# Kernel tuning notes

Measured on AMD Instinct MI355X. Metric: run time of the kernel, lower is better.

Reference implementation:

```python
import jax, jax.numpy as jnp
import numpy as np

B, T, C = 4, 2048, 2048  # batch, n_target, n_context
KEY_SIZE = 1024
VALUE_SIZE = 1024
NUM_HEADS = 16
KEY_HIDDEN = 64
HEAD_SIZE = VALUE_SIZE // NUM_HEADS  # 64
NORMALISE = True


def setup_inputs() -> dict:
    key = jax.random.key(0)
    ks = jax.random.split(key, 7)
    s = 0.02
    return {
        "queries": jax.random.normal(ks[0], (B, T, KEY_SIZE), jnp.float32),
        "keys": jax.random.normal(ks[1], (B, C, KEY_SIZE), jnp.float32),
        "values": jax.random.normal(ks[2], (B, C, VALUE_SIZE), jnp.float32),
        "Wq": jax.random.normal(ks[3], (NUM_HEADS * KEY_HIDDEN, KEY_SIZE), jnp.float32) * s,
        "Wk": jax.random.normal(ks[4], (NUM_HEADS * KEY_HIDDEN, KEY_SIZE), jnp.float32) * s,
        "Wv": jax.random.normal(ks[5], (NUM_HEADS * HEAD_SIZE, VALUE_SIZE), jnp.float32) * s,
        "Wo": jax.random.normal(ks[6], (VALUE_SIZE, NUM_HEADS * HEAD_SIZE), jnp.float32) * s,
    }


def reference(queries, keys, values, Wq, Wk, Wv, Wo):
    # Linear projections (torch nn.Linear: x @ W.T), reshape to heads
    q = (queries @ Wq.T).reshape(B, T, NUM_HEADS, KEY_HIDDEN)   # [B,T,H,Dk]
    k = (keys @ Wk.T).reshape(B, C, NUM_HEADS, KEY_HIDDEN)      # [B,C,H,Dk]
    v = (values @ Wv.T).reshape(B, C, NUM_HEADS, HEAD_SIZE)     # [B,C,H,Dv]
    scale = np.sqrt(KEY_HIDDEN).astype(np.float32)
    # Scores [B,H,T,C]
    scores = jnp.einsum('bthd,bchd->bhtc', q, k) / scale
    if NORMALISE:
        attn = jax.nn.softmax(scores, axis=-1)
    else:
        attn = jax.nn.sigmoid(scores)
    out = jnp.einsum('bhtc,bchd->bthd', attn, v)                # [B,T,H,Dv]
    out = out.reshape(B, T, NUM_HEADS * HEAD_SIZE)
    return out @ Wo.T                                            # [B,T,VALUE_SIZE]
```

## Files before the change

kernel.cpp:

```cpp
#include <hip/hip_runtime.h>
#include <stdint.h>

#define BATCH 4
#define SEQ   2048
#define EMB   1024
#define NH    16
#define HD    64

typedef __attribute__((ext_vector_type(4))) float  floatx4;
typedef __attribute__((ext_vector_type(8))) short  shortx8;

__device__ __forceinline__ unsigned short f2bf(float f) {
  unsigned u = __builtin_bit_cast(unsigned, f);
  u += 0x7FFFu + ((u >> 16) & 1u);
  return (unsigned short)(u >> 16);
}

__device__ __forceinline__ unsigned pack2bf(float a, float b) {
  return (unsigned)f2bf(a) | ((unsigned)f2bf(b) << 16);
}

__device__ __forceinline__ unsigned packtrunc(float a, float b) {
#if __has_builtin(__builtin_amdgcn_perm)
  return __builtin_amdgcn_perm(__builtin_bit_cast(unsigned, b),
                               __builtin_bit_cast(unsigned, a), 0x07060302u);
#else
  return (__builtin_bit_cast(unsigned, a) >> 16) |
         (__builtin_bit_cast(unsigned, b) & 0xFFFF0000u);
#endif
}

__device__ __forceinline__ float fexp2(float x) {
#if __has_builtin(__builtin_amdgcn_exp2f)
  return __builtin_amdgcn_exp2f(x);
#else
  return exp2f(x);
#endif
}

__device__ __forceinline__ void gl_lds16(const void* g, void* l) {
  __builtin_amdgcn_global_load_lds((const __attribute__((address_space(1))) void*)g,
                                   (__attribute__((address_space(3))) void*)l,
                                   16, 0, 0);
}

__device__ __forceinline__ void cast_body(const float* __restrict__ in,
                                          unsigned short* __restrict__ out, int bb, int t) {
  size_t i = (size_t)bb * 256 + t;
  const float4* p = (const float4*)in + i * 2;
  float4 f0 = p[0], f1 = p[1];
  uint4 o;
  o.x = pack2bf(f0.x, f0.y);
  o.y = pack2bf(f0.z, f0.w);
  o.z = pack2bf(f1.x, f1.y);
  o.w = pack2bf(f1.z, f1.w);
  ((uint4*)out)[i] = o;
}

__global__ __launch_bounds__(256) void cast_bf16(const float* __restrict__ in,
                                                 unsigned short* __restrict__ out) {
  cast_body(in, out, blockIdx.x, threadIdx.x);
}

__global__ __launch_bounds__(256) void cast_all(
    const float* __restrict__ q, const float* __restrict__ k, const float* __restrict__ v,
    const float* __restrict__ w0, const float* __restrict__ w1,
    const float* __restrict__ w2, const float* __restrict__ w3,
    unsigned short* __restrict__ oq, unsigned short* __restrict__ ok, unsigned short* __restrict__ ov,
    unsigned short* __restrict__ ow0, unsigned short* __restrict__ ow1,
    unsigned short* __restrict__ ow2, unsigned short* __restrict__ ow3) {
  int bb = blockIdx.x;
  const float* in; unsigned short* out;
  if      (bb < 4096)  { in = q;  out = oq; }
  else if (bb < 8192)  { in = k;  out = ok;  bb -= 4096; }
  else if (bb < 12288) { in = v;  out = ov;  bb -= 8192; }
  else if (bb < 12800) { in = w0; out = ow0; bb -= 12288; }
  else if (bb < 13312) { in = w1; out = ow1; bb -= 12800; }
  else if (bb < 13824) { in = w2; out = ow2; bb -= 13312; }
  else                 { in = w3; out = ow3; bb -= 13824; }
  cast_body(in, out, bb, threadIdx.x);
}

__global__ __launch_bounds__(256) void cast_w4(const float* __restrict__ i0, const float* __restrict__ i1,
                                               const float* __restrict__ i2, const float* __restrict__ i3,
                                               unsigned short* __restrict__ o0, unsigned short* __restrict__ o1,
                                               unsigned short* __restrict__ o2, unsigned short* __restrict__ o3) {
  int bb = blockIdx.x;
  const float* in; unsigned short* out;
  if      (bb < 512)  { in = i0; out = o0; }
  else if (bb < 1024) { in = i1; out = o1; bb -= 512; }
  else if (bb < 1536) { in = i2; out = o2; bb -= 1024; }
  else                { in = i3; out = o3; bb -= 1536; }
  cast_body(in, out, bb, threadIdx.x);
}

#define TST 136
template <int MODE>
__device__ __forceinline__ void gemm_body(const unsigned short* __restrict__ A,
                                          const unsigned short* __restrict__ Bt,
                                          void* __restrict__ Cp, float cscale,
                                          unsigned short* As, unsigned short* Bs,
                                          unsigned short* Ts) {
  constexpr int N = EMB, K = EMB;
  constexpr int BM = 128, BN = 128, BK = 64;
  const int t = threadIdx.x, w = t >> 6, lane = t & 63;
  const int quad = lane >> 4, lrow = lane & 15;
  const int m0 = blockIdx.y * BM, n0 = blockIdx.x * BN;
  const int wm = (w >> 1) * 64, wn = (w & 1) * 64;
  floatx4 acc[4][4] = {};

  const unsigned short* asrc[4];
  const unsigned short* bsrc[4];
#pragma unroll
  for (int i = 0; i < 4; i++) {
    int q = i * 256 + t;
    int r = q >> 3, kc = (q & 7) ^ (r & 7);
    asrc[i] = A + (size_t)(m0 + r) * K + kc * 8;
    bsrc[i] = Bt + (size_t)(n0 + r) * K + kc * 8;
  }

  for (int k0 = 0; k0 < K; k0 += BK) {
#pragma unroll
    for (int i = 0; i < 4; i++) {
      gl_lds16(asrc[i], (char*)As + (size_t)(i * 256 + w * 64) * 16);
      gl_lds16(bsrc[i], (char*)Bs + (size_t)(i * 256 + w * 64) * 16);
      asrc[i] += BK; bsrc[i] += BK;
    }
    __syncthreads();
#pragma unroll
    for (int ks = 0; ks < 2; ks++) {
      shortx8 a[4];
#pragma unroll
      for (int mi = 0; mi < 4; mi++) {
        int row = wm + mi * 16 + lrow;
        a[mi] = *(const shortx8*)(As + row * 64 + (((ks * 4 + quad) ^ (row & 7)) * 8));
      }
#pragma unroll
      for (int ni = 0; ni < 4; ni++) {
        int rowb = wn + ni * 16 + lrow;
        shortx8 b = *(const shortx8*)(Bs + rowb * 64 + (((ks * 4 + quad) ^ (rowb & 7)) * 8));
#pragma unroll
        for (int mi = 0; mi < 4; mi++)
          acc[mi][ni] = __builtin_amdgcn_mfma_f32_16x16x32_bf16(a[mi], b, acc[mi][ni], 0, 0, 0);
      }
    }
    __syncthreads();
  }

  if constexpr (MODE == 2) {
#pragma unroll
    for (int u = 0; u < 2; u++)
#pragma unroll
      for (int ni = 0; ni < 4; ni++) {
        uint4 p;
        p.x = pack2bf(acc[2 * u][ni][0], acc[2 * u + 1][ni][0]);
        p.y = pack2bf(acc[2 * u][ni][1], acc[2 * u + 1][ni][1]);
        p.z = pack2bf(acc[2 * u][ni][2], acc[2 * u + 1][ni][2]);
        p.w = pack2bf(acc[2 * u][ni][3], acc[2 * u + 1][ni][3]);
        int col = wn + ni * 16 + lrow;
        int cloc = wm + u * 32 + quad * 8;
        *(uint4*)(Ts + col * TST + cloc) = p;
      }
    __syncthreads();
    unsigned short* vTout = (unsigned short*)Cp;
    const int b = m0 >> 11, cbase = m0 & 2047, h0 = n0 >> 6;
#pragma unroll
    for (int i = 0; i < 8; i++) {
      int g = t + 256 * i;
      int hh2 = g >> 10, d = (g >> 4) & 63, a = g & 15;
      uint4 v = *(const uint4*)(Ts + (hh2 * 64 + d) * TST + a * 8);
      *(uint4*)(vTout + ((size_t)((b * NH + h0 + hh2) * HD + d)) * SEQ + cbase + a * 8) = v;
    }
    __syncthreads();
  } else {
#pragma unroll
    for (int mi = 0; mi < 4; mi++)
#pragma unroll
      for (int ni = 0; ni < 4; ni++)
#pragma unroll
        for (int r = 0; r < 4; r++) {
          int row = m0 + wm + mi * 16 + quad * 4 + r;
          int col = n0 + wn + ni * 16 + lrow;
          float v = acc[mi][ni][r] * cscale;
          if constexpr (MODE == 1) ((float*)Cp)[(size_t)row * N + col] = v;
          else                     ((unsigned short*)Cp)[(size_t)row * N + col] = f2bf(v);
        }
  }
}

__global__ __launch_bounds__(256, 2) void gemm_qk(
    const unsigned short* __restrict__ Xq, const unsigned short* __restrict__ Xk,
    const unsigned short* __restrict__ Wq, const unsigned short* __restrict__ Wk,
    unsigned short* __restrict__ Oq, unsigned short* __restrict__ Ok, float sq) {
  __shared__ unsigned short As[128 * 64];
  __shared__ unsigned short Bs[128 * 64];
  if (blockIdx.z == 0) gemm_body<0>(Xq, Wq, Oq, sq,   As, Bs, nullptr);
  else                 gemm_body<0>(Xk, Wk, Ok, 1.0f, As, Bs, nullptr);
}

__global__ __launch_bounds__(256, 2) void gemm_b(const unsigned short* __restrict__ A,
                                                 const unsigned short* __restrict__ Bt,
                                                 unsigned short* __restrict__ C, float sc) {
  __shared__ unsigned short As[128 * 64];
  __shared__ unsigned short Bs[128 * 64];
  gemm_body<0>(A, Bt, C, sc, As, Bs, nullptr);
}
__global__ __launch_bounds__(256, 2) void gemm_vt(const unsigned short* __restrict__ A,
                                                  const unsigned short* __restrict__ Bt,
                                                  unsigned short* __restrict__ C) {
  __shared__ unsigned short As[128 * 64];
  __shared__ unsigned short Bs[128 * 64];
  __shared__ unsigned short Ts[128 * TST];
  gemm_body<2>(A, Bt, C, 1.0f, As, Bs, Ts);
}
__global__ __launch_bounds__(256, 2) void gemm_o(const unsigned short* __restrict__ A,
                                                 const unsigned short* __restrict__ Bt,
                                                 float* __restrict__ C) {
  __shared__ unsigned short As[128 * 64];
  __shared__ unsigned short Bs[128 * 64];
  gemm_body<1>(A, Bt, C, 1.0f, As, Bs, nullptr);
}

__global__ __launch_bounds__(256, 4) void flash_attn(const unsigned short* __restrict__ qp,
                                                     const unsigned short* __restrict__ kp,
                                                     const unsigned short* __restrict__ vT,
                                                     unsigned short* __restrict__ ao) {
  __shared__ unsigned short Ks[2][64 * 64];
  __shared__ unsigned short Vts[2][64 * 64];
  __shared__ unsigned short Ps[4][16 * 40];
  const int h = blockIdx.x & (NH - 1), b = blockIdx.x >> 4;
  const int t0 = blockIdx.y * 128;
  const int t = threadIdx.x, w = t >> 6, lane = t & 63;
  const int quad = lane >> 4, lrow = lane & 15;

  shortx8 qfrag[2][2];
#pragma unroll
  for (int kk = 0; kk < 2; kk++)
#pragma unroll
    for (int mi = 0; mi < 2; mi++) {
      int row = w * 32 + mi * 16 + lrow;
      qfrag[kk][mi] = *(const shortx8*)(qp + ((size_t)(b * SEQ + t0 + row)) * EMB +
                                        h * HD + kk * 32 + quad * 8);
    }

  const unsigned short* ksrc[2];
  const unsigned short* vsrc[2];
#pragma unroll
  for (int i = 0; i < 2; i++) {
    int p = i * 256 + t;
    int r = p >> 3, kc = (p & 7) ^ (r & 7);
    ksrc[i] = kp + ((size_t)(b * SEQ + r)) * EMB + h * HD + kc * 8;
    vsrc[i] = vT + ((size_t)((b * NH + h) * HD + r)) * SEQ + kc * 8;
  }

  float l_st[2][4] = {};
  floatx4 accO[2][4] = {};

#pragma unroll
  for (int i = 0; i < 2; i++) {
    gl_lds16(ksrc[i], (char*)Ks[0] + (size_t)(i * 256 + w * 64) * 16);
    gl_lds16(vsrc[i], (char*)Vts[0] + (size_t)(i * 256 + w * 64) * 16);
    ksrc[i] += 64 * EMB;
    vsrc[i] += 64;
  }
  __syncthreads();

  for (int c0 = 0; c0 < SEQ; c0 += 64) {
    const int cur = (c0 >> 6) & 1;
    const unsigned short* Kc = Ks[cur];
    const unsigned short* Vc = Vts[cur];

    if (c0 + 64 < SEQ) {
#pragma unroll
      for (int i = 0; i < 2; i++) {
        gl_lds16(ksrc[i], (char*)Ks[cur ^ 1] + (size_t)(i * 256 + w * 64) * 16);
        gl_lds16(vsrc[i], (char*)Vts[cur ^ 1] + (size_t)(i * 256 + w * 64) * 16);
        ksrc[i] += 64 * EMB;
        vsrc[i] += 64;
      }
    }

    floatx4 accS[2][4] = {};
    __builtin_amdgcn_s_setprio(1);
#pragma unroll
    for (int kk = 0; kk < 2; kk++) {
      int qk = quad + kk * 4;
#pragma unroll
      for (int ni = 0; ni < 4; ni++) {
        int rowb = ni * 16 + lrow;
        shortx8 bfr = *(const shortx8*)(Kc + rowb * 64 + ((qk ^ (rowb & 7)) * 8));
#pragma unroll
        for (int mi = 0; mi < 2; mi++)
          accS[mi][ni] = __builtin_amdgcn_mfma_f32_16x16x32_bf16(qfrag[kk][mi], bfr, accS[mi][ni], 0, 0, 0);
      }
    }
    __builtin_amdgcn_s_setprio(0);

#pragma unroll
    for (int hh = 0; hh < 2; hh++) {
      shortx8 pafr[2];
#pragma unroll
      for (int mi = 0; mi < 2; mi++) {
#pragma unroll
        for (int r = 0; r < 4; r++) {
          float p0 = fexp2(accS[mi][2 * hh][r]);
          float p1 = fexp2(accS[mi][2 * hh + 1][r]);
          l_st[mi][r] += p0 + p1;
          *(unsigned*)(&Ps[w][(quad * 4 + r) * 40 + lrow * 2]) = packtrunc(p0, p1);
        }
        pafr[mi] = *(const shortx8*)(&Ps[w][lrow * 40 + quad * 8]);
      }
      __builtin_amdgcn_s_setprio(1);
#pragma unroll
      for (int nio = 0; nio < 4; nio++) {
        int d = nio * 16 + lrow;
        shortx8 bfr = *(const shortx8*)(Vc + d * 64 + ((((hh << 2) + quad) ^ (d & 7)) * 8));
#pragma unroll
        for (int mi = 0; mi < 2; mi++)
          accO[mi][nio] = __builtin_amdgcn_mfma_f32_16x16x32_bf16(pafr[mi], bfr, accO[mi][nio], 0, 0, 0);
      }
      __builtin_amdgcn_s_setprio(0);
    }

    __syncthreads();
  }

#pragma unroll
  for (int mi = 0; mi < 2; mi++)
#pragma unroll
    for (int r = 0; r < 4; r++) {
      float l = l_st[mi][r];
      l += __shfl_xor(l, 1);
      l += __shfl_xor(l, 2);
      l += __shfl_xor(l, 4);
      l += __shfl_xor(l, 8);
      float inv = 1.0f / l;
#pragma unroll
      for (int nio = 0; nio < 4; nio++) accO[mi][nio][r] *= inv;
    }
#pragma unroll
  for (int mi = 0; mi < 2; mi++)
#pragma unroll
    for (int nio = 0; nio < 4; nio++)
#pragma unroll
      for (int r = 0; r < 4; r++) {
        int row = t0 + w * 32 + mi * 16 + quad * 4 + r;
        int col = h * HD + nio * 16 + lrow;
        ao[((size_t)(b * SEQ + row)) * EMB + col] = f2bf(accO[mi][nio][r]);
      }
}

extern "C" void kernel_launch(void* const* d_in, const int* in_sizes, int n_in,
                              void* d_out, int out_size, void* d_ws, size_t ws_size,
                              hipStream_t stream) {
  const float* queries = (const float*)d_in[0];
  const float* keys    = (const float*)d_in[1];
  const float* values  = (const float*)d_in[2];
  const float* Wq      = (const float*)d_in[3];
  const float* Wk      = (const float*)d_in[4];
  const float* Wv      = (const float*)d_in[5];
  const float* Wo      = (const float*)d_in[6];

  char* ws = (char*)d_ws;
  const size_t MB = 1ull << 20;
  const float SC2 = 0.125f * 1.44269504088896341f;

  unsigned short* wq_b = (unsigned short*)(ws + 0 * MB);
  unsigned short* wk_b = (unsigned short*)(ws + 2 * MB);
  unsigned short* wv_b = (unsigned short*)(ws + 4 * MB);
  unsigned short* wo_b = (unsigned short*)(ws + 6 * MB);

  dim3 gg(EMB / 128, (BATCH * SEQ) / 128);
  dim3 fg(NH * BATCH, SEQ / 128);

  if (ws_size >= 104 * MB) {
    unsigned short* Xq = (unsigned short*)(ws + 8 * MB);
    unsigned short* Xk = (unsigned short*)(ws + 24 * MB);
    unsigned short* Xv = (unsigned short*)(ws + 40 * MB);
    unsigned short* qp = (unsigned short*)(ws + 56 * MB);
    unsigned short* kp = (unsigned short*)(ws + 72 * MB);
    unsigned short* vT = (unsigned short*)(ws + 88 * MB);
    unsigned short* ao = Xq;

    cast_all<<<14336, 256, 0, stream>>>(queries, keys, values, Wq, Wk, Wv, Wo,
                                        Xq, Xk, Xv, wq_b, wk_b, wv_b, wo_b);
    gemm_qk<<<dim3(gg.x, gg.y, 2), 256, 0, stream>>>(Xq, Xk, wq_b, wk_b, qp, kp, SC2);
    gemm_vt<<<gg, 256, 0, stream>>>(Xv, wv_b, vT);
    flash_attn<<<fg, 256, 0, stream>>>(qp, kp, vT, ao);
    gemm_o<<<gg, 256, 0, stream>>>(ao, wo_b, (float*)d_out);
  } else {
    unsigned short* X  = (unsigned short*)(ws + 8 * MB);
    unsigned short* qp = (unsigned short*)(ws + 24 * MB);
    unsigned short* kp = (unsigned short*)(ws + 40 * MB);
    unsigned short* vT = (unsigned short*)(ws + 56 * MB);
    unsigned short* ao = X;

    cast_w4<<<2048, 256, 0, stream>>>(Wq, Wk, Wv, Wo, wq_b, wk_b, wv_b, wo_b);
    cast_bf16<<<4096, 256, 0, stream>>>(queries, X);
    gemm_b<<<gg, 256, 0, stream>>>(X, wq_b, qp, SC2);
    cast_bf16<<<4096, 256, 0, stream>>>(keys, X);
    gemm_b<<<gg, 256, 0, stream>>>(X, wk_b, kp, 1.0f);
    cast_bf16<<<4096, 256, 0, stream>>>(values, X);
    gemm_vt<<<gg, 256, 0, stream>>>(X, wv_b, vT);
    flash_attn<<<fg, 256, 0, stream>>>(qp, kp, vT, ao);
    gemm_o<<<gg, 256, 0, stream>>>(ao, wo_b, (float*)d_out);
  }
}
```

Before: 325.0 us.

## Software-pipeline PV matmul one tile behind QK with triple-buffered V

Restructures the flash-attention loop so the P·V MFMAs for the previous K/V tile are issued after the current tile's Q·K^T. The packed P fragments are held in registers across iterations, and V gets a third LDS buffer, rotated through pointers, so the delayed tile stays resident. The goal is to overlap the exp/softmax VALU work with MFMA work and break the dependency between S and PV. In exchange it adds VGPRs for the carried P fragments and more LDS, and the occupancy hint drops from 4 to 3 blocks per CU.

```diff
diff --git a/kernel.cpp b/kernel.cpp
--- a/kernel.cpp
+++ b/kernel.cpp
@@ -221,12 +221,12 @@
   gemm_body<1>(A, Bt, C, 1.0f, As, Bs, nullptr);
 }
 
-__global__ __launch_bounds__(256, 4) void flash_attn(const unsigned short* __restrict__ qp,
+__global__ __launch_bounds__(256, 3) void flash_attn(const unsigned short* __restrict__ qp,
                                                      const unsigned short* __restrict__ kp,
                                                      const unsigned short* __restrict__ vT,
                                                      unsigned short* __restrict__ ao) {
   __shared__ unsigned short Ks[2][64 * 64];
-  __shared__ unsigned short Vts[2][64 * 64];
+  __shared__ unsigned short Vts[3][64 * 64];
   __shared__ unsigned short Ps[4][16 * 40];
   const int h = blockIdx.x & (NH - 1), b = blockIdx.x >> 4;
   const int t0 = blockIdx.y * 128;
@@ -255,30 +255,32 @@
 
   float l_st[2][4] = {};
   floatx4 accO[2][4] = {};
+  shortx8 pafr_c[2][2];
+
+  unsigned short* vp0 = Vts[0];
+  unsigned short* vp1 = Vts[1];
+  unsigned short* vp2 = Vts[2];
 
 #pragma unroll
   for (int i = 0; i < 2; i++) {
     gl_lds16(ksrc[i], (char*)Ks[0] + (size_t)(i * 256 + w * 64) * 16);
-    gl_lds16(vsrc[i], (char*)Vts[0] + (size_t)(i * 256 + w * 64) * 16);
+    gl_lds16(vsrc[i], (char*)vp0 + (size_t)(i * 256 + w * 64) * 16);
     ksrc[i] += 64 * EMB;
     vsrc[i] += 64;
   }
   __syncthreads();
 
-  for (int c0 = 0; c0 < SEQ; c0 += 64) {
-    const int cur = (c0 >> 6) & 1;
-    const unsigned short* Kc = Ks[cur];
-    const unsigned short* Vc = Vts[cur];
-
-    if (c0 + 64 < SEQ) {
+  for (int it = 0; it < SEQ / 64; ++it) {
+    if (it + 1 < SEQ / 64) {
 #pragma unroll
       for (int i = 0; i < 2; i++) {
-        gl_lds16(ksrc[i], (char*)Ks[cur ^ 1] + (size_t)(i * 256 + w * 64) * 16);
-        gl_lds16(vsrc[i], (char*)Vts[cur ^ 1] + (size_t)(i * 256 + w * 64) * 16);
+        gl_lds16(ksrc[i], (char*)Ks[(it + 1) & 1] + (size_t)(i * 256 + w * 64) * 16);
+        gl_lds16(vsrc[i], (char*)vp1 + (size_t)(i * 256 + w * 64) * 16);
         ksrc[i] += 64 * EMB;
         vsrc[i] += 64;
       }
     }
+    const unsigned short* Kc = Ks[it & 1];
 
     floatx4 accS[2][4] = {};
     __builtin_amdgcn_s_setprio(1);
@@ -296,9 +298,23 @@
     }
     __builtin_amdgcn_s_setprio(0);
 
-#pragma unroll
-    for (int hh = 0; hh < 2; hh++) {
-      shortx8 pafr[2];
+    if (it > 0) {
+      __builtin_amdgcn_s_setprio(1);
+#pragma unroll
+      for (int hh = 0; hh < 2; hh++)
+#pragma unroll
+        for (int nio = 0; nio < 4; nio++) {
+          int d = nio * 16 + lrow;
+          shortx8 bfr = *(const shortx8*)(vp2 + d * 64 + ((((hh << 2) + quad) ^ (d & 7)) * 8));
+#pragma unroll
+          for (int mi = 0; mi < 2; mi++)
+            accO[mi][nio] = __builtin_amdgcn_mfma_f32_16x16x32_bf16(pafr_c[hh][mi], bfr, accO[mi][nio], 0, 0, 0);
+        }
+      __builtin_amdgcn_s_setprio(0);
+    }
+
+#pragma unroll
+    for (int hh = 0; hh < 2; hh++)
 #pragma unroll
       for (int mi = 0; mi < 2; mi++) {
 #pragma unroll
@@ -308,22 +324,24 @@
           l_st[mi][r] += p0 + p1;
           *(unsigned*)(&Ps[w][(quad * 4 + r) * 40 + lrow * 2]) = packtrunc(p0, p1);
         }
-        pafr[mi] = *(const shortx8*)(&Ps[w][lrow * 40 + quad * 8]);
-      }
-      __builtin_amdgcn_s_setprio(1);
-#pragma unroll
-      for (int nio = 0; nio < 4; nio++) {
-        int d = nio * 16 + lrow;
-        shortx8 bfr = *(const shortx8*)(Vc + d * 64 + ((((hh << 2) + quad) ^ (d & 7)) * 8));
-#pragma unroll
-        for (int mi = 0; mi < 2; mi++)
-          accO[mi][nio] = __builtin_amdgcn_mfma_f32_16x16x32_bf16(pafr[mi], bfr, accO[mi][nio], 0, 0, 0);
-      }
-      __builtin_amdgcn_s_setprio(0);
-    }
+        pafr_c[hh][mi] = *(const shortx8*)(&Ps[w][lrow * 40 + quad * 8]);
+      }
 
     __syncthreads();
-  }
+
+    unsigned short* vtmp = vp0; vp0 = vp1; vp1 = vp2; vp2 = vtmp;
+  }
+
+#pragma unroll
+  for (int hh = 0; hh < 2; hh++)
+#pragma unroll
+    for (int nio = 0; nio < 4; nio++) {
+      int d = nio * 16 + lrow;
+      shortx8 bfr = *(const shortx8*)(vp2 + d * 64 + ((((hh << 2) + quad) ^ (d & 7)) * 8));
+#pragma unroll
+      for (int mi = 0; mi < 2; mi++)
+        accO[mi][nio] = __builtin_amdgcn_mfma_f32_16x16x32_bf16(pafr_c[hh][mi], bfr, accO[mi][nio], 0, 0, 0);
+    }
 
 #pragma unroll
   for (int mi = 0; mi < 2; mi++)
```

Result: slower. 355.6 us (+9.4%).
